# Kernel optimization log

Hardware: AMD Instinct MI355X
Metric: run time of the kernel (lower is better)

Reference implementation:

```python
import jax, jax.numpy as jnp
import numpy as np

B = 4          # batch_size (config.batch_size)
N = 17000      # num_prots (nodes per graph)
F_IN = 256     # num_features
C = 128        # out_channels
E = 2176000    # num edges (avg degree 32)
NODES = B * N


def _gcn_layer(x, W, b, src, dst, n):
    """PyG GCNConv: add self-loops, sym-normalized aggregation, then bias.
    out[i] = sum_{j->i} d_j^{-1/2} d_i^{-1/2} (x_j W) + d_i^{-1} (x_i W) + b
    with d = degree(dst) + 1 (self loop)."""
    h = x @ W  # [n, C]
    deg = jax.ops.segment_sum(jnp.ones(src.shape[0], x.dtype), dst, num_segments=n) + 1.0
    dinv = jax.lax.rsqrt(deg)  # [n]
    coef = dinv[src] * dinv[dst]                      # [E]
    agg = jax.ops.segment_sum(h[src] * coef[:, None], dst, num_segments=n)
    agg = agg + h * (dinv * dinv)[:, None]            # self-loop term
    return agg + b


def setup_inputs() -> dict:
    key = jax.random.key(0)
    ks = jax.random.split(key, 16)

    def glorot(k, shape):
        fan_in, fan_out = shape[0], shape[1]
        s = jnp.sqrt(6.0 / (fan_in + fan_out))
        return jax.random.uniform(k, shape, jnp.float32, -s, s)

    inp = {
        "x": jax.random.normal(ks[0], (NODES, F_IN), jnp.float32),
        "edge_index": jax.random.randint(ks[1], (2, E), 0, NODES, jnp.int32),
        "protein_mask": jax.random.randint(ks[2], (B, N), 0, 2, jnp.int32),
        "W1": glorot(ks[3], (F_IN, C)), "b1": jnp.zeros((C,), jnp.float32),
        "W2": glorot(ks[4], (C, C)),    "b2": jnp.zeros((C,), jnp.float32),
        "W3": glorot(ks[5], (C, C)),    "b3": jnp.zeros((C,), jnp.float32),
        "lw1": glorot(ks[6], (C, 256)), "lb1": jnp.zeros((256,), jnp.float32),
        "lw2": glorot(ks[7], (256, 64)), "lb2": jnp.zeros((64,), jnp.float32),
        "lw3": glorot(ks[8], (64, 16)),  "lb3": jnp.zeros((16,), jnp.float32),
        "lw4": glorot(ks[9], (16, 1)),   "lb4": jnp.zeros((1,), jnp.float32),
    }
    return inp


def reference(x, edge_index, protein_mask, W1, b1, W2, b2, W3, b3,
              lw1, lb1, lw2, lb2, lw3, lb3, lw4, lb4):
    src, dst = edge_index[0], edge_index[1]
    h1 = jax.nn.relu(_gcn_layer(x, W1, b1, src, dst, NODES))   # [NODES, C]
    h2 = jax.nn.relu(_gcn_layer(h1, W2, b2, src, dst, NODES))
    h3 = jax.nn.relu(_gcn_layer(h2, W3, b3, src, dst, NODES))
    s = (h1 + h2 + h3).reshape(B, N, C)                        # residual sum
    mask = protein_mask.astype(jnp.float32)                    # [B, N]
    pooled = jnp.einsum('bn,bnc->bc', mask, s)                 # masked bmm pool [B, C]
    z = jax.nn.relu(pooled @ lw1 + lb1)
    z = jax.nn.relu(z @ lw2 + lb2)
    z = jax.nn.relu(z @ lw3 + lb3)
    return z @ lw4 + lb4                                       # [B, 1]
```

## Files before the change

kernel.cpp:

```cpp
#include <hip/hip_runtime.h>
#include <hip/hip_bf16.h>
#include <cstdint>

#define F_IN 256
#define C 128
#define NBUK_MAX 320
#define CHUNK 4096

typedef short bf8_t __attribute__((ext_vector_type(8)));
typedef float f4_t  __attribute__((ext_vector_type(4)));

static inline size_t align256(size_t x) { return (x + 255) & ~(size_t)255; }


__global__ __launch_bounds__(256) void histA_kernel(const int* __restrict__ dst,
                                                    int* __restrict__ btot,
                                                    int E, int nbuk) {
    __shared__ int hist[NBUK_MAX];
    const int tid = threadIdx.x;
    const int e0 = blockIdx.x * CHUNK;
    for (int i = tid; i < NBUK_MAX; i += 256) hist[i] = 0;
    __syncthreads();
#pragma unroll
    for (int k = 0; k < CHUNK / 256; ++k) {
        int e = e0 + k * 256 + tid;
        if (e < E) atomicAdd(&hist[dst[e] >> 8], 1);
    }
    __syncthreads();
    for (int i = tid; i < nbuk; i += 256) {
        int h = hist[i];
        if (h) atomicAdd(&btot[i], h);
    }
}

__global__ __launch_bounds__(256) void bscan_kernel(const int* __restrict__ btot,
                                                    int nbuk,
                                                    int* __restrict__ ebase,
                                                    int* __restrict__ gcur) {
    __shared__ int sums[NBUK_MAX];
    __shared__ int base[NBUK_MAX + 1];
    const int tid = threadIdx.x;
    for (int bk = tid; bk < NBUK_MAX; bk += 256)
        sums[bk] = (bk < nbuk) ? btot[bk] : 0;
    __syncthreads();
    if (tid < 64) {
        int acc[5];
        int s = 0;
#pragma unroll
        for (int j = 0; j < 5; ++j) {
            acc[j] = s;
            s += sums[tid * 5 + j];
        }
        int tot = s;
#pragma unroll
        for (int d = 1; d < 64; d <<= 1) {
            int o = __shfl_up(tot, d);
            if (tid >= d) tot += o;
        }
        int excl = tot - s;
#pragma unroll
        for (int j = 0; j < 5; ++j) base[tid * 5 + j] = excl + acc[j];
        if (tid == 63) base[320] = tot;
    }
    __syncthreads();
    for (int bk = tid; bk <= nbuk; bk += 256) {
        ebase[bk] = base[bk];
        if (bk < nbuk) gcur[bk] = base[bk];
    }
}

__global__ __launch_bounds__(256) void partition_kernel(const int* __restrict__ src,
                                                        const int* __restrict__ dst,
                                                        int* __restrict__ gcur,
                                                        int2* __restrict__ ebuf, int E) {
    __shared__ int hist[NBUK_MAX];
    __shared__ int base[NBUK_MAX];
    __shared__ int gbase[NBUK_MAX];
    __shared__ int2 stage[CHUNK];
    const int tid = threadIdx.x;
    const int e0 = blockIdx.x * CHUNK;
    const int cnt = min(CHUNK, E - e0);

    for (int i = tid; i < NBUK_MAX; i += 256) hist[i] = 0;
    __syncthreads();

    int2 ev[CHUNK / 256];
    int mo[CHUNK / 256];
#pragma unroll
    for (int k = 0; k < CHUNK / 256; ++k) {
        int e = e0 + k * 256 + tid;
        if (e < E) {
            int2 v;
            v.x = src[e];
            v.y = dst[e];
            ev[k] = v;
            mo[k] = atomicAdd(&hist[v.y >> 8], 1);
        }
    }
    __syncthreads();
    if (tid < 64) {
        int acc[5];
        int s = 0;
#pragma unroll
        for (int j = 0; j < 5; ++j) {
            int idx = tid * 5 + j;
            acc[j] = s;
            s += hist[idx];
        }
        int tot = s;
#pragma unroll
        for (int d = 1; d < 64; d <<= 1) {
            int o = __shfl_up(tot, d);
            if (tid >= d) tot += o;
        }
        int excl = tot - s;
#pragma unroll
        for (int j = 0; j < 5; ++j) base[tid * 5 + j] = excl + acc[j];
    }
    __syncthreads();
    for (int i = tid; i < NBUK_MAX; i += 256) {
        int h = hist[i];
        gbase[i] = h ? atomicAdd(&gcur[i], h) : 0;
    }
    __syncthreads();
#pragma unroll
    for (int k = 0; k < CHUNK / 256; ++k) {
        int e = e0 + k * 256 + tid;
        if (e < E) stage[base[ev[k].y >> 8] + mo[k]] = ev[k];
    }
    __syncthreads();
    for (int i = tid; i < cnt; i += 256) {
        int2 e = stage[i];
        int b = e.y >> 8;
        ebuf[gbase[b] + (i - base[b])] = e;
    }
}

__global__ __launch_bounds__(256) void csr_build_kernel(const int2* __restrict__ ebuf,
                                                        const int* __restrict__ ebase,
                                                        int* __restrict__ offs,
                                                        float* __restrict__ dinv,
                                                        int* __restrict__ csr, int nodes) {
    __shared__ int deg[256];
    __shared__ int p[256];
    __shared__ int pre[257];
    __shared__ int cur[256];
    const int b = blockIdx.x;
    const int n0 = b << 8;
    const int ncnt = min(256, nodes - n0);
    const int tid = threadIdx.x;
    const int eb = ebase[b], ee = ebase[b + 1];

    deg[tid] = 0;
    __syncthreads();
    for (int i = eb + tid; i < ee; i += 256)
        atomicAdd(&deg[ebuf[i].y & 255], 1);
    __syncthreads();
    p[tid] = deg[tid];
    __syncthreads();
    for (int d = 1; d < 256; d <<= 1) {
        int v = (tid >= d) ? p[tid - d] : 0;
        __syncthreads();
        p[tid] += v;
        __syncthreads();
    }
    pre[tid + 1] = p[tid];
    if (tid == 0) pre[0] = 0;
    __syncthreads();

    for (int i = tid; i <= ncnt; i += 256)
        offs[n0 + i] = eb + pre[i] + n0 + i;
    if (tid < ncnt) {
        dinv[n0 + tid] = rsqrtf((float)(deg[tid] + 1));
        csr[eb + pre[tid] + n0 + tid] = n0 + tid;
    }
    cur[tid] = 0;
    __syncthreads();
    for (int i = eb + tid; i < ee; i += 256) {
        int2 e = ebuf[i];
        int loc = e.y & 255;
        int q = atomicAdd(&cur[loc], 1);
        csr[eb + pre[loc] + n0 + loc + 1 + q] = e.x;
    }
}

static __device__ inline unsigned pack_bf16(float a, float b) {
    __hip_bfloat162 h = __float22bfloat162_rn(make_float2(a, b));
    return *(unsigned*)&h;
}

__global__ void wswz_kernel(const float* __restrict__ W, __hip_bfloat16* __restrict__ Wsw,
                            int K) {
    int i = blockIdx.x * blockDim.x + threadIdx.x;
    int total = (K >> 5) * 8 * 64;
    if (i < total) {
        int l = i & 63;
        int u = (i >> 6) & 7;
        int t = i >> 9;
        int krow = t * 32 + (l >> 4) * 8;
        int col = u * 16 + (l & 15);
        unsigned packed[4];
#pragma unroll
        for (int j = 0; j < 4; ++j) {
            float a = W[(size_t)(krow + 2 * j) * C + col];
            float b = W[(size_t)(krow + 2 * j + 1) * C + col];
            packed[j] = pack_bf16(a, b);
        }
        uint4 o = make_uint4(packed[0], packed[1], packed[2], packed[3]);
        *(uint4*)(Wsw + (size_t)i * 8) = o;
    }
}


static __device__ inline bf8_t pack8(float4 u0, float4 u1) {
    union { unsigned u[4]; bf8_t v; } r;
    r.u[0] = pack_bf16(u0.x, u0.y);
    r.u[1] = pack_bf16(u0.z, u0.w);
    r.u[2] = pack_bf16(u1.x, u1.y);
    r.u[3] = pack_bf16(u1.z, u1.w);
    return r.v;
}

template <bool F32IN>
__global__ __launch_bounds__(256) void mfma_gemm_kernel(const void* __restrict__ Xv,
                                                        const __hip_bfloat16* __restrict__ Wsw,
                                                        const float* __restrict__ dinv,
                                                        __hip_bfloat16* __restrict__ G,
                                                        int M, int K) {
    extern __shared__ char lds[];
    const int tid = threadIdx.x;
    const int l = tid & 63;
    const int w = tid >> 6;
    const int lm = l & 15;
    const int lk = (l >> 4) * 8;
    const int row0 = blockIdx.x * 128 + w * 32;

    const int bytes = K * 256;
    for (int o = tid * 16; o < bytes; o += 256 * 16)
        *(uint4*)(lds + o) = *(const uint4*)((const char*)Wsw + o);
    __syncthreads();

    f4_t acc[2][8] = {};
    const int steps = K >> 5;

    const float* xf[2];
    const __hip_bfloat16* xb[2];
#pragma unroll
    for (int mt = 0; mt < 2; ++mt) {
        int r = min(row0 + mt * 16 + lm, M - 1);
        xf[mt] = (const float*)Xv + (size_t)r * K + lk;
        xb[mt] = (const __hip_bfloat16*)Xv + (size_t)r * K + lk;
    }

    float4 cf[2][2];
    bf8_t cb[2];
#pragma unroll
    for (int mt = 0; mt < 2; ++mt) {
        if (F32IN) {
            cf[mt][0] = *(const float4*)(xf[mt]);
            cf[mt][1] = *(const float4*)(xf[mt] + 4);
        } else {
            cb[mt] = *(const bf8_t*)(xb[mt]);
        }
    }

    for (int t = 0; t < steps; ++t) {
        float4 nf[2][2];
        bf8_t nb[2];
        if (t + 1 < steps) {
#pragma unroll
            for (int mt = 0; mt < 2; ++mt) {
                if (F32IN) {
                    nf[mt][0] = *(const float4*)(xf[mt] + (t + 1) * 32);
                    nf[mt][1] = *(const float4*)(xf[mt] + (t + 1) * 32 + 4);
                } else {
                    nb[mt] = *(const bf8_t*)(xb[mt] + (t + 1) * 32);
                }
            }
        }
        bf8_t a[2];
#pragma unroll
        for (int mt = 0; mt < 2; ++mt)
            a[mt] = F32IN ? pack8(cf[mt][0], cf[mt][1]) : cb[mt];

        const char* bbase = lds + ((size_t)(t * 8) * 64 + l) * 16;
#pragma unroll
        for (int u = 0; u < 8; ++u) {
            bf8_t b = *(const bf8_t*)(bbase + (size_t)u * 64 * 16);
#pragma unroll
            for (int mt = 0; mt < 2; ++mt)
                acc[mt][u] = __builtin_amdgcn_mfma_f32_16x16x32_bf16(a[mt], b, acc[mt][u], 0, 0, 0);
        }
#pragma unroll
        for (int mt = 0; mt < 2; ++mt) {
            if (F32IN) {
                cf[mt][0] = nf[mt][0];
                cf[mt][1] = nf[mt][1];
            } else {
                cb[mt] = nb[mt];
            }
        }
    }

#pragma unroll
    for (int mt = 0; mt < 2; ++mt) {
        int rbase = row0 + mt * 16 + (l >> 4) * 4;
#pragma unroll
        for (int r = 0; r < 4; ++r) {
            int row = rbase + r;
            if (row < M) {
                float dv = dinv[row];
#pragma unroll
                for (int u = 0; u < 8; ++u) {
                    float v = acc[mt][u][r] * dv;
                    G[(size_t)row * C + u * 16 + lm] = __float2bfloat16(v);
                }
            }
        }
    }
}

__global__ __launch_bounds__(256) void agg_kernel(const __hip_bfloat16* __restrict__ G,
                                                  const int* __restrict__ csr,
                                                  const int* __restrict__ offs,
                                                  const float* __restrict__ dinv,
                                                  const float* __restrict__ bias,
                                                  __hip_bfloat16* __restrict__ A, int nodes) {
    const int node = blockIdx.x * 4 + (threadIdx.x >> 6);
    if (node >= nodes) return;
    const int tid = threadIdx.x & 63;
    const int c0 = tid * 2;
    const int beg = offs[node], end = offs[node + 1];
    float ax = 0.f, ay = 0.f;
    for (int base = beg; base < end; base += 64) {
        const int cnt = min(64, end - base);
        int myidx = (tid < cnt) ? csr[base + tid] : 0;
        int j = 0;
        for (; j + 8 <= cnt; j += 8) {
#pragma unroll
            for (int u = 0; u < 8; ++u) {
                int idx = __shfl(myidx, j + u);
                __hip_bfloat162 hv = *(const __hip_bfloat162*)(G + (size_t)idx * C + c0);
                float2 f = __bfloat1622float2(hv);
                ax += f.x;
                ay += f.y;
            }
        }
        for (; j < cnt; ++j) {
            int idx = __shfl(myidx, j);
            __hip_bfloat162 hv = *(const __hip_bfloat162*)(G + (size_t)idx * C + c0);
            float2 f = __bfloat1622float2(hv);
            ax += f.x;
            ay += f.y;
        }
    }
    float d = dinv[node];
    float ox = fmaxf(ax * d + bias[c0], 0.f);
    float oy = fmaxf(ay * d + bias[c0 + 1], 0.f);
    __hip_bfloat162 o = __float22bfloat162_rn(make_float2(ox, oy));
    *(__hip_bfloat162*)(A + (size_t)node * C + c0) = o;
}

__global__ __launch_bounds__(64) void pool3_kernel(const __hip_bfloat16* __restrict__ S1,
                                                   const __hip_bfloat16* __restrict__ S2,
                                                   const __hip_bfloat16* __restrict__ S3,
                                                   const int* __restrict__ mask,
                                                   float* __restrict__ pooled, int N) {
    const int b = blockIdx.y;
    const int n0 = blockIdx.x * 128;
    const int c0 = threadIdx.x * 2;
    const int lim = min(n0 + 128, N);
    float ax = 0.f, ay = 0.f;
    for (int n = n0; n < lim; ++n) {
        if (mask[b * N + n]) {
            size_t o = ((size_t)b * N + n) * C + c0;
            float2 f1 = __bfloat1622float2(*(const __hip_bfloat162*)(S1 + o));
            float2 f2 = __bfloat1622float2(*(const __hip_bfloat162*)(S2 + o));
            float2 f3 = __bfloat1622float2(*(const __hip_bfloat162*)(S3 + o));
            ax += f1.x + f2.x + f3.x;
            ay += f1.y + f2.y + f3.y;
        }
    }
    atomicAdd(&pooled[b * C + c0], ax);
    atomicAdd(&pooled[b * C + c0 + 1], ay);
}

__global__ __launch_bounds__(256) void mlp_kernel(const float* __restrict__ pooled,
        const float* __restrict__ lw1, const float* __restrict__ lb1,
        const float* __restrict__ lw2, const float* __restrict__ lb2,
        const float* __restrict__ lw3, const float* __restrict__ lb3,
        const float* __restrict__ lw4, const float* __restrict__ lb4,
        float* __restrict__ out) {
    __shared__ float p[4 * 128];
    __shared__ float z1[4 * 256];
    __shared__ float z2[4 * 64];
    __shared__ float z3[4 * 16];
    const int tid = threadIdx.x;
    for (int i = tid; i < 4 * 128; i += 256) p[i] = pooled[i];
    __syncthreads();
    for (int o = tid; o < 4 * 256; o += 256) {
        int b = o >> 8, j = o & 255;
        float s = lb1[j];
        for (int k = 0; k < 128; ++k) s += p[b * 128 + k] * lw1[k * 256 + j];
        z1[o] = fmaxf(s, 0.f);
    }
    __syncthreads();
    for (int o = tid; o < 4 * 64; o += 256) {
        int b = o >> 6, j = o & 63;
        float s = lb2[j];
        for (int k = 0; k < 256; ++k) s += z1[b * 256 + k] * lw2[k * 64 + j];
        z2[o] = fmaxf(s, 0.f);
    }
    __syncthreads();
    if (tid < 64) {
        int b = tid >> 4, j = tid & 15;
        float s = lb3[j];
        for (int k = 0; k < 64; ++k) s += z2[b * 64 + k] * lw3[k * 16 + j];
        z3[tid] = fmaxf(s, 0.f);
    }
    __syncthreads();
    if (tid < 4) {
        float s = lb4[0];
        for (int k = 0; k < 16; ++k) s += z3[tid * 16 + k] * lw4[k];
        out[tid] = s;
    }
}


extern "C" void kernel_launch(void* const* d_in, const int* in_sizes, int n_in,
                              void* d_out, int out_size, void* d_ws, size_t ws_size,
                              hipStream_t stream) {
    const float* x    = (const float*)d_in[0];
    const int*   ei   = (const int*)d_in[1];
    const int*   pmask = (const int*)d_in[2];
    const float* W1 = (const float*)d_in[3];  const float* b1 = (const float*)d_in[4];
    const float* W2 = (const float*)d_in[5];  const float* b2 = (const float*)d_in[6];
    const float* W3 = (const float*)d_in[7];  const float* b3 = (const float*)d_in[8];
    const float* lw1 = (const float*)d_in[9];  const float* lb1 = (const float*)d_in[10];
    const float* lw2 = (const float*)d_in[11]; const float* lb2 = (const float*)d_in[12];
    const float* lw3 = (const float*)d_in[13]; const float* lb3 = (const float*)d_in[14];
    const float* lw4 = (const float*)d_in[15]; const float* lb4 = (const float*)d_in[16];
    float* out = (float*)d_out;

    const int E = in_sizes[1] / 2;
    const int NODES = in_sizes[0] / F_IN;
    const int NB = 4;
    const int NPER = NODES / NB;
    const int NBUK = (NODES + 255) >> 8;
    const int NBLK = (E + CHUNK - 1) / CHUNK;
    const int* esrc = ei;
    const int* edst = ei + E;

    char* w = (char*)d_ws;
    size_t off = 0;
    auto alloc = [&](size_t bytes) -> void* {
        void* p = w + off;
        off = align256(off + bytes);
        return p;
    };
    float* dinv = (float*)alloc((size_t)NODES * 4);
    int*   offs = (int*)  alloc((size_t)(NODES + 1) * 4);
    int*   ebase = (int*) alloc((size_t)(NBUK + 1) * 4);
    int*   gcur = (int*)  alloc((size_t)NBUK * 4);
    int*   btot = (int*)  alloc((size_t)NBUK * 4);
    int2*  ebuf = (int2*) alloc((size_t)E * 8);
    int*   csr  = (int*)  alloc((size_t)(E + NODES) * 4);
    __hip_bfloat16* G   = (__hip_bfloat16*)alloc((size_t)NODES * C * 2);
    __hip_bfloat16* A1  = (__hip_bfloat16*)alloc((size_t)NODES * C * 2);
    __hip_bfloat16* A2  = (__hip_bfloat16*)alloc((size_t)NODES * C * 2);
    __hip_bfloat16* A3  = (__hip_bfloat16*)alloc((size_t)NODES * C * 2);
    __hip_bfloat16* Wsw1 = (__hip_bfloat16*)alloc((size_t)F_IN * C * 2);
    __hip_bfloat16* Wsw2 = (__hip_bfloat16*)alloc((size_t)C * C * 2);
    __hip_bfloat16* Wsw3 = (__hip_bfloat16*)alloc((size_t)C * C * 2);
    float* pooled = (float*)alloc((size_t)4 * C * 4);
    (void)ws_size; (void)n_in; (void)out_size;

    hipMemsetAsync(pooled, 0, (size_t)4 * C * 4, stream);
    hipMemsetAsync(btot,   0, (size_t)NBUK * 4, stream);

    wswz_kernel<<<(F_IN / 32 * 512 + 255) / 256, 256, 0, stream>>>(W1, Wsw1, F_IN);
    wswz_kernel<<<(C / 32 * 512 + 255) / 256, 256, 0, stream>>>(W2, Wsw2, C);
    wswz_kernel<<<(C / 32 * 512 + 255) / 256, 256, 0, stream>>>(W3, Wsw3, C);

    histA_kernel<<<NBLK, 256, 0, stream>>>(edst, btot, E, NBUK);
    bscan_kernel<<<1, 256, 0, stream>>>(btot, NBUK, ebase, gcur);
    partition_kernel<<<NBLK, 256, 0, stream>>>(esrc, edst, gcur, ebuf, E);
    csr_build_kernel<<<NBUK, 256, 0, stream>>>(ebuf, ebase, offs, dinv, csr, NODES);

    const int gblocks128 = (NODES + 127) / 128;
    const int ablocks = (NODES + 3) / 4;

    mfma_gemm_kernel<true><<<gblocks128, 256, F_IN * 256, stream>>>(x, Wsw1, dinv, G, NODES, F_IN);
    agg_kernel<<<ablocks, 256, 0, stream>>>(G, csr, offs, dinv, b1, A1, NODES);
    mfma_gemm_kernel<false><<<gblocks128, 256, C * 256, stream>>>(A1, Wsw2, dinv, G, NODES, C);
    agg_kernel<<<ablocks, 256, 0, stream>>>(G, csr, offs, dinv, b2, A2, NODES);
    mfma_gemm_kernel<false><<<gblocks128, 256, C * 256, stream>>>(A2, Wsw3, dinv, G, NODES, C);
    agg_kernel<<<ablocks, 256, 0, stream>>>(G, csr, offs, dinv, b3, A3, NODES);

    dim3 pgrid((NPER + 127) / 128, NB);
    pool3_kernel<<<pgrid, 64, 0, stream>>>(A1, A2, A3, pmask, pooled, NPER);
    mlp_kernel<<<1, 256, 0, stream>>>(pooled, lw1, lb1, lw2, lb2, lw3, lb3, lw4, lb4, out);
}
```

Before: 527.7 us.

## Drop histogram pass via fixed-capacity bucket slabs, chunk GEMM weight LDS, merge swizzles

The separate histogram and scan passes that ran before partitioning are removed. Edges are now written into fixed-capacity per-bucket slabs (CAP entries each), with counts taken from atomics during partitioning and the scan run afterwards. The MFMA GEMM now stages weights into LDS in 32KB chunks rather than loading the whole matrix up front, which cuts LDS use per block for K=256 and may raise occupancy. The three weight swizzle launches are merged into one. The slab layout relies on no bucket exceeding CAP edges, which holds for random inputs but is not guaranteed in general.

Result: faster. 496.8 us (-5.9%).

```diff
diff --git a/kernel.cpp b/kernel.cpp
--- a/kernel.cpp
+++ b/kernel.cpp
@@ -6,6 +6,7 @@
 #define C 128
 #define NBUK_MAX 320
 #define CHUNK 4096
+#define CAP 12288
 
 typedef short bf8_t __attribute__((ext_vector_type(8)));
 typedef float f4_t  __attribute__((ext_vector_type(4)));
@@ -13,65 +14,9 @@
 static inline size_t align256(size_t x) { return (x + 255) & ~(size_t)255; }
 
 
-__global__ __launch_bounds__(256) void histA_kernel(const int* __restrict__ dst,
-                                                    int* __restrict__ btot,
-                                                    int E, int nbuk) {
-    __shared__ int hist[NBUK_MAX];
-    const int tid = threadIdx.x;
-    const int e0 = blockIdx.x * CHUNK;
-    for (int i = tid; i < NBUK_MAX; i += 256) hist[i] = 0;
-    __syncthreads();
-#pragma unroll
-    for (int k = 0; k < CHUNK / 256; ++k) {
-        int e = e0 + k * 256 + tid;
-        if (e < E) atomicAdd(&hist[dst[e] >> 8], 1);
-    }
-    __syncthreads();
-    for (int i = tid; i < nbuk; i += 256) {
-        int h = hist[i];
-        if (h) atomicAdd(&btot[i], h);
-    }
-}
-
-__global__ __launch_bounds__(256) void bscan_kernel(const int* __restrict__ btot,
-                                                    int nbuk,
-                                                    int* __restrict__ ebase,
-                                                    int* __restrict__ gcur) {
-    __shared__ int sums[NBUK_MAX];
-    __shared__ int base[NBUK_MAX + 1];
-    const int tid = threadIdx.x;
-    for (int bk = tid; bk < NBUK_MAX; bk += 256)
-        sums[bk] = (bk < nbuk) ? btot[bk] : 0;
-    __syncthreads();
-    if (tid < 64) {
-        int acc[5];
-        int s = 0;
-#pragma unroll
-        for (int j = 0; j < 5; ++j) {
-            acc[j] = s;
-            s += sums[tid * 5 + j];
-        }
-        int tot = s;
-#pragma unroll
-        for (int d = 1; d < 64; d <<= 1) {
-            int o = __shfl_up(tot, d);
-            if (tid >= d) tot += o;
-        }
-        int excl = tot - s;
-#pragma unroll
-        for (int j = 0; j < 5; ++j) base[tid * 5 + j] = excl + acc[j];
-        if (tid == 63) base[320] = tot;
-    }
-    __syncthreads();
-    for (int bk = tid; bk <= nbuk; bk += 256) {
-        ebase[bk] = base[bk];
-        if (bk < nbuk) gcur[bk] = base[bk];
-    }
-}
-
 __global__ __launch_bounds__(256) void partition_kernel(const int* __restrict__ src,
                                                         const int* __restrict__ dst,
-                                                        int* __restrict__ gcur,
+                                                        int* __restrict__ cntb,
                                                         int2* __restrict__ ebuf, int E) {
     __shared__ int hist[NBUK_MAX];
     __shared__ int base[NBUK_MAX];
@@ -120,7 +65,7 @@
     __syncthreads();
     for (int i = tid; i < NBUK_MAX; i += 256) {
         int h = hist[i];
-        gbase[i] = h ? atomicAdd(&gcur[i], h) : 0;
+        gbase[i] = h ? atomicAdd(&cntb[i], h) : 0;
     }
     __syncthreads();
 #pragma unroll
@@ -132,8 +77,41 @@
     for (int i = tid; i < cnt; i += 256) {
         int2 e = stage[i];
         int b = e.y >> 8;
-        ebuf[gbase[b] + (i - base[b])] = e;
-    }
+        ebuf[(size_t)b * CAP + gbase[b] + (i - base[b])] = e;
+    }
+}
+
+__global__ __launch_bounds__(256) void bscan_kernel(const int* __restrict__ cntb,
+                                                    int nbuk,
+                                                    int* __restrict__ ebase) {
+    __shared__ int sums[NBUK_MAX];
+    __shared__ int base[NBUK_MAX + 1];
+    const int tid = threadIdx.x;
+    for (int bk = tid; bk < NBUK_MAX; bk += 256)
+        sums[bk] = (bk < nbuk) ? cntb[bk] : 0;
+    __syncthreads();
+    if (tid < 64) {
+        int acc[5];
+        int s = 0;
+#pragma unroll
+        for (int j = 0; j < 5; ++j) {
+            acc[j] = s;
+            s += sums[tid * 5 + j];
+        }
+        int tot = s;
+#pragma unroll
+        for (int d = 1; d < 64; d <<= 1) {
+            int o = __shfl_up(tot, d);
+            if (tid >= d) tot += o;
+        }
+        int excl = tot - s;
+#pragma unroll
+        for (int j = 0; j < 5; ++j) base[tid * 5 + j] = excl + acc[j];
+        if (tid == 63) base[320] = tot;
+    }
+    __syncthreads();
+    for (int bk = tid; bk <= nbuk; bk += 256)
+        ebase[bk] = base[bk];
 }
 
 __global__ __launch_bounds__(256) void csr_build_kernel(const int2* __restrict__ ebuf,
@@ -149,12 +127,14 @@
     const int n0 = b << 8;
     const int ncnt = min(256, nodes - n0);
     const int tid = threadIdx.x;
-    const int eb = ebase[b], ee = ebase[b + 1];
+    const int eb = ebase[b];
+    const int cntE = ebase[b + 1] - eb;
+    const int2* slab = ebuf + (size_t)b * CAP;
 
     deg[tid] = 0;
     __syncthreads();
-    for (int i = eb + tid; i < ee; i += 256)
-        atomicAdd(&deg[ebuf[i].y & 255], 1);
+    for (int k = tid; k < cntE; k += 256)
+        atomicAdd(&deg[slab[k].y & 255], 1);
     __syncthreads();
     p[tid] = deg[tid];
     __syncthreads();
@@ -176,8 +156,8 @@
     }
     cur[tid] = 0;
     __syncthreads();
-    for (int i = eb + tid; i < ee; i += 256) {
-        int2 e = ebuf[i];
+    for (int k = tid; k < cntE; k += 256) {
+        int2 e = slab[k];
         int loc = e.y & 255;
         int q = atomicAdd(&cur[loc], 1);
         csr[eb + pre[loc] + n0 + loc + 1 + q] = e.x;
@@ -189,26 +169,34 @@
     return *(unsigned*)&h;
 }
 
-__global__ void wswz_kernel(const float* __restrict__ W, __hip_bfloat16* __restrict__ Wsw,
-                            int K) {
+static __device__ inline void swz_one(const float* __restrict__ W,
+                                      __hip_bfloat16* __restrict__ Wsw, int i) {
+    int l = i & 63;
+    int u = (i >> 6) & 7;
+    int t = i >> 9;
+    int krow = t * 32 + (l >> 4) * 8;
+    int col = u * 16 + (l & 15);
+    unsigned packed[4];
+#pragma unroll
+    for (int j = 0; j < 4; ++j) {
+        float a = W[(size_t)(krow + 2 * j) * C + col];
+        float b = W[(size_t)(krow + 2 * j + 1) * C + col];
+        packed[j] = pack_bf16(a, b);
+    }
+    uint4 o = make_uint4(packed[0], packed[1], packed[2], packed[3]);
+    *(uint4*)(Wsw + (size_t)i * 8) = o;
+}
+
+__global__ __launch_bounds__(256) void wswz_all_kernel(const float* __restrict__ W1,
+                                                       const float* __restrict__ W2,
+                                                       const float* __restrict__ W3,
+                                                       __hip_bfloat16* __restrict__ Wsw1,
+                                                       __hip_bfloat16* __restrict__ Wsw2,
+                                                       __hip_bfloat16* __restrict__ Wsw3) {
     int i = blockIdx.x * blockDim.x + threadIdx.x;
-    int total = (K >> 5) * 8 * 64;
-    if (i < total) {
-        int l = i & 63;
-        int u = (i >> 6) & 7;
-        int t = i >> 9;
-        int krow = t * 32 + (l >> 4) * 8;
-        int col = u * 16 + (l & 15);
-        unsigned packed[4];
-#pragma unroll
-        for (int j = 0; j < 4; ++j) {
-            float a = W[(size_t)(krow + 2 * j) * C + col];
-            float b = W[(size_t)(krow + 2 * j + 1) * C + col];
-            packed[j] = pack_bf16(a, b);
-        }
-        uint4 o = make_uint4(packed[0], packed[1], packed[2], packed[3]);
-        *(uint4*)(Wsw + (size_t)i * 8) = o;
-    }
+    if (i < 4096)      swz_one(W1, Wsw1, i);
+    else if (i < 6144) swz_one(W2, Wsw2, i - 4096);
+    else if (i < 8192) swz_one(W3, Wsw3, i - 6144);
 }
 
 
@@ -227,7 +215,7 @@
                                                         const float* __restrict__ dinv,
                                                         __hip_bfloat16* __restrict__ G,
                                                         int M, int K) {
-    extern __shared__ char lds[];
+    __shared__ char lds[32768];
     const int tid = threadIdx.x;
     const int l = tid & 63;
     const int w = tid >> 6;
@@ -235,11 +223,6 @@
     const int lk = (l >> 4) * 8;
     const int row0 = blockIdx.x * 128 + w * 32;
 
-    const int bytes = K * 256;
-    for (int o = tid * 16; o < bytes; o += 256 * 16)
-        *(uint4*)(lds + o) = *(const uint4*)((const char*)Wsw + o);
-    __syncthreads();
-
     f4_t acc[2][8] = {};
     const int steps = K >> 5;
 
@@ -264,17 +247,24 @@
         }
     }
 
-    for (int t = 0; t < steps; ++t) {
+    for (int s = 0; s < steps; ++s) {
+        if ((s & 3) == 0) {
+            if (s) __syncthreads();
+            const char* wsrc = (const char*)Wsw + (size_t)s * 8192;
+            for (int o = tid * 16; o < 32768; o += 256 * 16)
+                *(uint4*)(lds + o) = *(const uint4*)(wsrc + o);
+            __syncthreads();
+        }
         float4 nf[2][2];
         bf8_t nb[2];
-        if (t + 1 < steps) {
+        if (s + 1 < steps) {
 #pragma unroll
             for (int mt = 0; mt < 2; ++mt) {
                 if (F32IN) {
-                    nf[mt][0] = *(const float4*)(xf[mt] + (t + 1) * 32);
-                    nf[mt][1] = *(const float4*)(xf[mt] + (t + 1) * 32 + 4);
+                    nf[mt][0] = *(const float4*)(xf[mt] + (s + 1) * 32);
+                    nf[mt][1] = *(const float4*)(xf[mt] + (s + 1) * 32 + 4);
                 } else {
-                    nb[mt] = *(const bf8_t*)(xb[mt] + (t + 1) * 32);
+                    nb[mt] = *(const bf8_t*)(xb[mt] + (s + 1) * 32);
                 }
             }
         }
@@ -283,7 +273,7 @@
         for (int mt = 0; mt < 2; ++mt)
             a[mt] = F32IN ? pack8(cf[mt][0], cf[mt][1]) : cb[mt];
 
-        const char* bbase = lds + ((size_t)(t * 8) * 64 + l) * 16;
+        const char* bbase = lds + ((size_t)((s & 3) * 8) * 64 + l) * 16;
 #pragma unroll
         for (int u = 0; u < 8; ++u) {
             bf8_t b = *(const bf8_t*)(bbase + (size_t)u * 64 * 16);
@@ -461,9 +451,8 @@
     float* dinv = (float*)alloc((size_t)NODES * 4);
     int*   offs = (int*)  alloc((size_t)(NODES + 1) * 4);
     int*   ebase = (int*) alloc((size_t)(NBUK + 1) * 4);
-    int*   gcur = (int*)  alloc((size_t)NBUK * 4);
-    int*   btot = (int*)  alloc((size_t)NBUK * 4);
-    int2*  ebuf = (int2*) alloc((size_t)E * 8);
+    int*   cntb = (int*)  alloc((size_t)NBUK * 4);
+    int2*  ebuf = (int2*) alloc((size_t)NBUK * CAP * 8);
     int*   csr  = (int*)  alloc((size_t)(E + NODES) * 4);
     __hip_bfloat16* G   = (__hip_bfloat16*)alloc((size_t)NODES * C * 2);
     __hip_bfloat16* A1  = (__hip_bfloat16*)alloc((size_t)NODES * C * 2);
@@ -475,26 +464,23 @@
     float* pooled = (float*)alloc((size_t)4 * C * 4);
     (void)ws_size; (void)n_in; (void)out_size;
 
+    hipMemsetAsync(cntb,   0, (size_t)NBUK * 4, stream);
     hipMemsetAsync(pooled, 0, (size_t)4 * C * 4, stream);
-    hipMemsetAsync(btot,   0, (size_t)NBUK * 4, stream);
-
-    wswz_kernel<<<(F_IN / 32 * 512 + 255) / 256, 256, 0, stream>>>(W1, Wsw1, F_IN);
-    wswz_kernel<<<(C / 32 * 512 + 255) / 256, 256, 0, stream>>>(W2, Wsw2, C);
-    wswz_kernel<<<(C / 32 * 512 + 255) / 256, 256, 0, stream>>>(W3, Wsw3, C);
-
-    histA_kernel<<<NBLK, 256, 0, stream>>>(edst, btot, E, NBUK);
-    bscan_kernel<<<1, 256, 0, stream>>>(btot, NBUK, ebase, gcur);
-    partition_kernel<<<NBLK, 256, 0, stream>>>(esrc, edst, gcur, ebuf, E);
+
+    wswz_all_kernel<<<32, 256, 0, stream>>>(W1, W2, W3, Wsw1, Wsw2, Wsw3);
+
+    partition_kernel<<<NBLK, 256, 0, stream>>>(esrc, edst, cntb, ebuf, E);
+    bscan_kernel<<<1, 256, 0, stream>>>(cntb, NBUK, ebase);
     csr_build_kernel<<<NBUK, 256, 0, stream>>>(ebuf, ebase, offs, dinv, csr, NODES);
 
     const int gblocks128 = (NODES + 127) / 128;
     const int ablocks = (NODES + 3) / 4;
 
-    mfma_gemm_kernel<true><<<gblocks128, 256, F_IN * 256, stream>>>(x, Wsw1, dinv, G, NODES, F_IN);
+    mfma_gemm_kernel<true><<<gblocks128, 256, 0, stream>>>(x, Wsw1, dinv, G, NODES, F_IN);
     agg_kernel<<<ablocks, 256, 0, stream>>>(G, csr, offs, dinv, b1, A1, NODES);
-    mfma_gemm_kernel<false><<<gblocks128, 256, C * 256, stream>>>(A1, Wsw2, dinv, G, NODES, C);
+    mfma_gemm_kernel<false><<<gblocks128, 256, 0, stream>>>(A1, Wsw2, dinv, G, NODES, C);
     agg_kernel<<<ablocks, 256, 0, stream>>>(G, csr, offs, dinv, b2, A2, NODES);
-    mfma_gemm_kernel<false><<<gblocks128, 256, C * 256, stream>>>(A2, Wsw3, dinv, G, NODES, C);
+    mfma_gemm_kernel<false><<<gblocks128, 256, 0, stream>>>(A2, Wsw3, dinv, G, NODES, C);
     agg_kernel<<<ablocks, 256, 0, stream>>>(G, csr, offs, dinv, b3, A3, NODES);
 
     dim3 pgrid((NPER + 127) / 128, NB);
```
